# Kernel optimization log

Hardware: AMD Instinct MI355X
Metric: run time of the kernel (lower is better)

Reference implementation:

```python
import jax, jax.numpy as jnp
import numpy as np

H = 1024      # hidden_size
NH = 16       # num_attention_heads
HD = H // NH  # attention_head_size = 64
B, S = 2, 2048


def setup_inputs() -> dict:
    key = jax.random.key(0)
    ks = jax.random.split(key, 8)
    scale = 1.0 / np.sqrt(H)
    return {
        "hidden_states": jax.random.normal(ks[0], (B, S, H), dtype=jnp.float32),
        "attention_mask": jnp.zeros((B, 1, 1, S), dtype=jnp.float32),
        "Wq": jax.random.normal(ks[1], (H, H), dtype=jnp.float32) * scale,
        "bq": jax.random.normal(ks[2], (H,), dtype=jnp.float32) * 0.02,
        "Wk": jax.random.normal(ks[3], (H, H), dtype=jnp.float32) * scale,
        "bk": jax.random.normal(ks[4], (H,), dtype=jnp.float32) * 0.02,
        "Wv": jax.random.normal(ks[5], (H, H), dtype=jnp.float32) * scale,
        "bv": jax.random.normal(ks[6], (H,), dtype=jnp.float32) * 0.02,
    }


def _split_heads(x):
    # [B,S,H] -> [B,NH,S,HD]
    b, s, _ = x.shape
    return x.reshape(b, s, NH, HD).transpose(0, 2, 1, 3)


def reference(hidden_states, attention_mask, Wq, bq, Wk, bk, Wv, bv):
    q = _split_heads(hidden_states @ Wq.T + bq)  # [B,NH,S,HD]
    k = _split_heads(hidden_states @ Wk.T + bk)
    v = _split_heads(hidden_states @ Wv.T + bv)
    scores = jnp.einsum("bhqd,bhkd->bhqk", q, k) / np.sqrt(HD).astype(np.float32)
    scores = scores + attention_mask  # additive mask, broadcast over heads/queries
    weights = jax.nn.softmax(scores, axis=-1)  # dropout is identity in eval mode
    ctx = jnp.einsum("bhqk,bhkd->bhqd", weights, v)  # [B,NH,S,HD]
    return ctx.transpose(0, 2, 1, 3).reshape(hidden_states.shape[0], hidden_states.shape[1], H)
```

## Files before the change

kernel.cpp:

```cpp
#include <hip/hip_runtime.h>
#include <hip/hip_bf16.h>
#include <math.h>

#define HSZ   1024
#define NHEAD 16
#define HDIM  64
#define BATCH 2
#define SEQ   2048

#define LOG2E 1.4426950408889634f

typedef __attribute__((ext_vector_type(8))) short short8;
typedef __attribute__((ext_vector_type(4))) short short4_t;
typedef __attribute__((ext_vector_type(4))) float floatx4;

typedef __attribute__((address_space(1))) const unsigned int gu32;
typedef __attribute__((address_space(3))) unsigned int lu32;

__device__ __forceinline__ void g2lds16(const void* g, void* l) {
    __builtin_amdgcn_global_load_lds((gu32*)g, (lu32*)l, 16, 0, 0);
}

__device__ __forceinline__ short f2bf(float f) {
    union { float f; unsigned u; } v; v.f = f;
    unsigned r = (v.u + 0x7FFF + ((v.u >> 16) & 1)) >> 16;
    return (short)r;
}

__device__ __forceinline__ unsigned pk2(float a, float b) {
    __hip_bfloat162 h = __float22bfloat162_rn(make_float2(a, b));
    return *(unsigned*)&h;
}

__device__ __forceinline__ float ex2(float x) {
#if __has_builtin(__builtin_amdgcn_exp2f)
    return __builtin_amdgcn_exp2f(x);
#else
    return exp2f(x);
#endif
}

#if __has_builtin(__builtin_amdgcn_mfma_f32_16x16x16_bf16)
#define MFMA16(a, b, c) __builtin_amdgcn_mfma_f32_16x16x16_bf16(a, b, c, 0, 0, 0)
#else
#define MFMA16(a, b, c) __builtin_amdgcn_mfma_f32_16x16x16bf16_1k(a, b, c, 0, 0, 0)
#endif

__global__ __launch_bounds__(256) void convert_kernel(
    const float4* __restrict__ X, const float4* __restrict__ Wq,
    const float4* __restrict__ Wk, const float4* __restrict__ Wv,
    const float4* __restrict__ Mask,
    short4_t* __restrict__ Xb, short4_t* __restrict__ Wb,
    float4* __restrict__ Mw)
{
    int idx = blockIdx.x * 256 + threadIdx.x;
    if (idx >= 1835008) {
        int t = idx - 1835008;
        float4 f = Mask[t];
        float4 o;
        o.x = f.x * LOG2E; o.y = f.y * LOG2E;
        o.z = f.z * LOG2E; o.w = f.w * LOG2E;
        Mw[t] = o;
        return;
    }
    const float4* src; short4_t* dst;
    if (idx < 1048576) { src = X + idx; dst = Xb + idx; }
    else {
        int t = idx - 1048576;
        int sel = t >> 18;
        int wi  = t & 0x3FFFF;
        src = (sel == 0 ? Wq : sel == 1 ? Wk : Wv) + wi;
        dst = Wb + (sel << 18) + wi;
    }
    float4 f = *src;
    short4_t o;
    o.x = f2bf(f.x); o.y = f2bf(f.y); o.z = f2bf(f.z); o.w = f2bf(f.w);
    *dst = o;
}

__global__ __launch_bounds__(256, 3) void qkv_mfma_kernel(
    const short* __restrict__ Xb, const short* __restrict__ Wb,
    const float* __restrict__ bq, const float* __restrict__ bk,
    const float* __restrict__ bv,
    short* __restrict__ qo, short* __restrict__ ko, short* __restrict__ vT)
{
    __shared__ short Sm[128 * 136];
    short* As = Sm;
    short* Bs = Sm + 8192;

    const int tid  = threadIdx.x;
    const int lane = tid & 63;
    const int w    = tid >> 6;
    const int l    = lane & 15, quad = lane >> 4;
    const int gM   = blockIdx.y * 128;
    const int gN   = blockIdx.x * 128;
    const int wm   = (w >> 1) * 64, wn = (w & 1) * 64;
    const int ci   = lane >> 3, pb = lane & 7;

    floatx4 acc[4][4] = {};

    for (int kt = 0; kt < HSZ / 64; ++kt) {
        const int k0 = kt * 64;
        __syncthreads();
        #pragma unroll
        for (int u = 0; u < 4; ++u) {
            int c  = w * 4 + u;
            int r  = c * 8 + ci;
            int lb = pb ^ (r & 7);
            g2lds16(Xb + (size_t)(gM + r) * HSZ + k0 + lb * 8, &As[c * 512]);
            g2lds16(Wb + (size_t)(gN + r) * HSZ + k0 + lb * 8, &Bs[c * 512]);
        }
        __syncthreads();
        #pragma unroll
        for (int kk = 0; kk < 2; ++kk) {
            short8 a[4], b[4];
            #pragma unroll
            for (int i = 0; i < 4; ++i) {
                int m = wm + i * 16 + l;
                a[i] = *(const short8*)&As[m * 64 + (((quad + kk * 4) ^ (m & 7)) << 3)];
                int n = wn + i * 16 + l;
                b[i] = *(const short8*)&Bs[n * 64 + (((quad + kk * 4) ^ (n & 7)) << 3)];
            }
            #pragma unroll
            for (int i = 0; i < 4; ++i)
                #pragma unroll
                for (int j = 0; j < 4; ++j)
                    acc[i][j] = __builtin_amdgcn_mfma_f32_16x16x32_bf16(
                        a[i], b[j], acc[i][j], 0, 0, 0);
        }
    }

    const int mat = gN >> 10;
    const int bb = gM >> 11, ss0 = gM & (SEQ - 1);

    if (mat == 2) {
        __syncthreads();
        #pragma unroll
        for (int j = 0; j < 4; ++j) {
            int fl = wn + j * 16 + l;
            float bv_ = bv[(gN & 1023) + fl];
            #pragma unroll
            for (int i = 0; i < 4; ++i)
                #pragma unroll
                for (int r = 0; r < 4; ++r)
                    Sm[fl * 136 + wm + i * 16 + quad * 4 + r]
                        = f2bf(acc[i][j][r] + bv_);
        }
        __syncthreads();
        #pragma unroll
        for (int it = 0; it < 16; ++it) {
            int f = (tid >> 5) + it * 8;
            int c = (tid & 31) * 4;
            short4_t val = *(const short4_t*)&Sm[f * 136 + c];
            int nft = (gN & 1023) + f;
            int head = nft >> 6, d = nft & 63;
            *(short4_t*)&vT[(((size_t)(bb * NHEAD + head)) * HDIM + d) * SEQ
                            + ss0 + c] = val;
        }
        return;
    }

    const float* bias = (mat == 0) ? bq : bk;
    short* dst        = (mat == 0) ? qo : ko;
    const float qscale = (mat == 0) ? 0.125f * LOG2E : 1.0f;

    __syncthreads();
    #pragma unroll
    for (int j = 0; j < 4; ++j) {
        int fl = wn + j * 16 + l;
        float bb_ = bias[(gN & 1023) + fl];
        #pragma unroll
        for (int i = 0; i < 4; ++i)
            #pragma unroll
            for (int r = 0; r < 4; ++r)
                Sm[(wm + i * 16 + quad * 4 + r) * 136 + fl]
                    = f2bf((acc[i][j][r] + bb_) * qscale);
    }
    __syncthreads();
    #pragma unroll
    for (int it = 0; it < 8; ++it) {
        int row = (tid >> 4) + it * 16;
        int fc  = (tid & 15) * 8;
        short8 val = *(const short8*)&Sm[row * 136 + fc];
        int nft = (gN & 1023) + fc;
        int head = nft >> 6, d = nft & 63;
        *(short8*)&dst[(((size_t)(bb * NHEAD + head)) * SEQ + ss0 + row) * HDIM + d]
            = val;
    }
}

__global__ __launch_bounds__(256, 3) void attn_kernel(
    const short* __restrict__ Qg, const short* __restrict__ Kg,
    const short* __restrict__ VTg, const float* __restrict__ maskw,
    float* __restrict__ out)
{
    __shared__ alignas(16) short Sh[4][4096];
    __shared__ alignas(16) float Ms[2][64];
    __shared__ alignas(16) float Lx[4][4][16];

    const int tid  = threadIdx.x;
    const int lane = tid & 63;
    const int kh   = tid >> 6;
    const int l    = lane & 15, quad = lane >> 4;
    const int idx  = blockIdx.x;
    const int bh   = idx & 31;
    const int qt   = idx >> 5;
    const int batch = bh >> 4, head = bh & 15;
    const int ci = lane >> 3, pb = lane & 7;

    const short* Qb = Qg + ((size_t)bh * SEQ + qt * 64) * HDIM;
    const short* Kb = Kg + (size_t)bh * SEQ * HDIM;
    const short* Vb = VTg + (size_t)bh * HDIM * SEQ;
    const float* mrow = maskw + (size_t)batch * SEQ;

    short* Qst = (short*)&Sh[2][0];

    #pragma unroll
    for (int u = 0; u < 2; ++u) {
        int c = kh * 2 + u;
        int r = c * 8 + ci;
        int lb = pb ^ (r & 7);
        g2lds16(Qb + (size_t)r * HDIM + lb * 8, &Qst[c * 512]);
        g2lds16(Kb + (size_t)r * HDIM + lb * 8, &Sh[0][c * 512]);
        g2lds16(Vb + (size_t)r * SEQ + lb * 8, &Sh[1][c * 512]);
    }
    if (tid < 16) g2lds16(mrow + tid * 4, &Ms[0][0]);
    __syncthreads();

    short8 aq[4][2];
    #pragma unroll
    for (int n = 0; n < 4; ++n)
        #pragma unroll
        for (int kk = 0; kk < 2; ++kk) {
            int m = n * 16 + l;
            aq[n][kk] = *(const short8*)&Qst[m * 64
                          + (((quad + kk * 4) ^ (m & 7)) << 3)];
        }
    __syncthreads();

    #pragma unroll
    for (int u = 0; u < 2; ++u) {
        int c = kh * 2 + u;
        int r = c * 8 + ci;
        int lb = pb ^ (r & 7);
        g2lds16(Kb + (size_t)(64 + r) * HDIM + lb * 8, &Sh[2][c * 512]);
        g2lds16(Vb + (size_t)r * SEQ + 64 + lb * 8, &Sh[3][c * 512]);
    }
    if (tid < 16) g2lds16(mrow + 64 + tid * 4, &Ms[1][0]);

    const int akoff0 = (kh * 16 + l) * 64 + (((quad + 0) ^ ((kh * 16 + l) & 7)) << 3);
    const int akoff1 = (kh * 16 + l) * 64 + (((quad + 4) ^ ((kh * 16 + l) & 7)) << 3);
    const int blog   = kh * 2 + (quad >> 1);
    const int bhalf  = (quad & 1) * 4;

    short8 ak0 = *(const short8*)&Sh[0][akoff0];
    short8 ak1 = *(const short8*)&Sh[0][akoff1];
    short4_t bvf[4];
    #pragma unroll
    for (int nd = 0; nd < 4; ++nd) {
        int d = nd * 16 + l;
        bvf[nd] = *(const short4_t*)&Sh[1][d * 64 + ((blog ^ (d & 7)) << 3) + bhalf];
    }
    floatx4 s[4];
    {
        float4 mq = *(const float4*)&Ms[0][kh * 16 + quad * 4];
        floatx4 ini = {mq.x, mq.y, mq.z, mq.w};
        #pragma unroll
        for (int n = 0; n < 4; ++n) s[n] = ini;
        #pragma unroll
        for (int n = 0; n < 4; ++n) {
            s[n] = __builtin_amdgcn_mfma_f32_16x16x32_bf16(ak0, aq[n][0], s[n], 0, 0, 0);
            s[n] = __builtin_amdgcn_mfma_f32_16x16x32_bf16(ak1, aq[n][1], s[n], 0, 0, 0);
        }
    }

    floatx4 o[4][4] = {};
    float l_i[4] = {0.f, 0.f, 0.f, 0.f};

    for (int t = 0; t < 32; ++t) {
        short4_t ap[4];
        #pragma unroll
        for (int n = 0; n < 4; ++n) {
            s[n][0] = ex2(s[n][0]);
            s[n][1] = ex2(s[n][1]);
            s[n][2] = ex2(s[n][2]);
            s[n][3] = ex2(s[n][3]);
            l_i[n] += (s[n][0] + s[n][1]) + (s[n][2] + s[n][3]);
            union { unsigned u[2]; short4_t s4; } pu;
            pu.u[0] = pk2(s[n][0], s[n][1]);
            pu.u[1] = pk2(s[n][2], s[n][3]);
            ap[n] = pu.s4;
        }
        #pragma unroll
        for (int nq = 0; nq < 4; ++nq)
            #pragma unroll
            for (int nd = 0; nd < 4; ++nd)
                o[nq][nd] = MFMA16(ap[nq], bvf[nd], o[nq][nd]);

        if (t < 31) {
            __syncthreads();
            if (t < 30) {
                const int r0 = (t + 2) * 64;
                const int bd = t & 1;
                #pragma unroll
                for (int u = 0; u < 2; ++u) {
                    int c = kh * 2 + u;
                    int r = c * 8 + ci;
                    int lb = pb ^ (r & 7);
                    g2lds16(Kb + (size_t)(r0 + r) * HDIM + lb * 8,
                            &Sh[2 * bd][c * 512]);
                    g2lds16(Vb + (size_t)r * SEQ + r0 + lb * 8,
                            &Sh[2 * bd + 1][c * 512]);
                }
                if (tid < 16) g2lds16(mrow + r0 + tid * 4, &Ms[t & 1][0]);
            }
            const int bb = (t + 1) & 1;
            ak0 = *(const short8*)&Sh[2 * bb][akoff0];
            ak1 = *(const short8*)&Sh[2 * bb][akoff1];
            #pragma unroll
            for (int nd = 0; nd < 4; ++nd) {
                int d = nd * 16 + l;
                bvf[nd] = *(const short4_t*)&Sh[2 * bb + 1]
                              [d * 64 + ((blog ^ (d & 7)) << 3) + bhalf];
            }
            float4 mq = *(const float4*)&Ms[bb][kh * 16 + quad * 4];
            floatx4 ini = {mq.x, mq.y, mq.z, mq.w};
            #pragma unroll
            for (int n = 0; n < 4; ++n) s[n] = ini;
            #pragma unroll
            for (int n = 0; n < 4; ++n) {
                s[n] = __builtin_amdgcn_mfma_f32_16x16x32_bf16(ak0, aq[n][0], s[n], 0, 0, 0);
                s[n] = __builtin_amdgcn_mfma_f32_16x16x32_bf16(ak1, aq[n][1], s[n], 0, 0, 0);
            }
        }
    }

    #pragma unroll
    for (int n = 0; n < 4; ++n) {
        float v = l_i[n];
        v += __shfl_xor(v, 16);
        v += __shfl_xor(v, 32);
        l_i[n] = v;
    }
    float* r0buf = (float*)&Sh[0][0];
    float* r1buf = (float*)&Sh[2][0];
    __syncthreads();
    if (kh != 0 && lane < 16) {
        #pragma unroll
        for (int n = 0; n < 4; ++n) Lx[kh][n][lane] = l_i[n];
    }
    if (kh == 1 || kh == 3) {
        float* dstb = (kh == 1) ? r0buf : r1buf;
        #pragma unroll
        for (int nq = 0; nq < 4; ++nq)
            #pragma unroll
            for (int nd = 0; nd < 4; ++nd)
                *(floatx4*)&dstb[((nq * 4 + nd) * 64 + lane) * 4] = o[nq][nd];
    }
    __syncthreads();
    if (kh == 0 || kh == 2) {
        const float* srcb = (kh == 0) ? r0buf : r1buf;
        #pragma unroll
        for (int nq = 0; nq < 4; ++nq)
            #pragma unroll
            for (int nd = 0; nd < 4; ++nd)
                o[nq][nd] += *(const floatx4*)&srcb[((nq * 4 + nd) * 64 + lane) * 4];
    }
    __syncthreads();
    if (kh == 2) {
        #pragma unroll
        for (int nq = 0; nq < 4; ++nq)
            #pragma unroll
            for (int nd = 0; nd < 4; ++nd)
                *(floatx4*)&r0buf[((nq * 4 + nd) * 64 + lane) * 4] = o[nq][nd];
    }
    __syncthreads();
    if (kh == 0) {
        #pragma unroll
        for (int nq = 0; nq < 4; ++nq)
            #pragma unroll
            for (int nd = 0; nd < 4; ++nd)
                o[nq][nd] += *(const floatx4*)&r0buf[((nq * 4 + nd) * 64 + lane) * 4];
        float lf[4];
        #pragma unroll
        for (int n = 0; n < 4; ++n)
            lf[n] = l_i[n] + Lx[1][n][l] + Lx[2][n][l] + Lx[3][n][l];
        #pragma unroll
        for (int nq = 0; nq < 4; ++nq) {
            #pragma unroll
            for (int r = 0; r < 4; ++r) {
                float inv = 1.0f / __shfl(lf[nq], (lane & 48) + quad * 4 + r);
                int qrow = qt * 64 + nq * 16 + quad * 4 + r;
                #pragma unroll
                for (int nd = 0; nd < 4; ++nd)
                    out[((size_t)batch * SEQ + qrow) * HSZ + head * HDIM + nd * 16 + l]
                        = o[nq][nd][r] * inv;
            }
        }
    }
}

extern "C" void kernel_launch(void* const* d_in, const int* in_sizes, int n_in,
                              void* d_out, int out_size, void* d_ws, size_t ws_size,
                              hipStream_t stream) {
    const float* hs   = (const float*)d_in[0];
    const float* mask = (const float*)d_in[1];
    const float* Wq   = (const float*)d_in[2];
    const float* bq   = (const float*)d_in[3];
    const float* Wk   = (const float*)d_in[4];
    const float* bk   = (const float*)d_in[5];
    const float* Wv   = (const float*)d_in[6];
    const float* bv   = (const float*)d_in[7];
    float* out = (float*)d_out;

    short* Xb = (short*)d_ws;
    short* Wb = Xb + 4194304;
    short* qb = Wb + 3145728;
    short* kb = qb + 4194304;
    short* vT = kb + 4194304;
    float* Mw = (float*)(vT + 4194304);

    convert_kernel<<<7172, 256, 0, stream>>>(
        (const float4*)hs, (const float4*)Wq, (const float4*)Wk, (const float4*)Wv,
        (const float4*)mask, (short4_t*)Xb, (short4_t*)Wb, (float4*)Mw);

    dim3 g2(3 * HSZ / 128, BATCH * SEQ / 128);
    qkv_mfma_kernel<<<g2, 256, 0, stream>>>(Xb, Wb, bq, bk, bv, qb, kb, vT);

    attn_kernel<<<1024, 256, 0, stream>>>(qb, kb, vT, Mw, out);
}
```

Before: 173.6 us.

## Load K/V fragments directly from global into registers, dropping LDS staging

Removes the LDS double-buffered staging of K, V and mask tiles along with the per-iteration block barrier. Each wave now loads its own MFMA operand fragments straight from global memory into registers, prefetching the next tile one iteration ahead. This cuts barrier and LDS traffic but replaces wide coalesced 16-byte async copies with narrower, strided per-lane global loads, notably the short4 V^T loads that stride by SEQ. LDS now holds only the final cross-wave reduction buffer.

```diff
diff --git a/kernel.cpp b/kernel.cpp
--- a/kernel.cpp
+++ b/kernel.cpp
@@ -194,8 +194,7 @@
     const short* __restrict__ VTg, const float* __restrict__ maskw,
     float* __restrict__ out)
 {
-    __shared__ alignas(16) short Sh[4][4096];
-    __shared__ alignas(16) float Ms[2][64];
+    __shared__ alignas(16) float Cb[2][4096];
     __shared__ alignas(16) float Lx[4][4][16];
 
     const int tid  = threadIdx.x;
@@ -206,78 +205,58 @@
     const int bh   = idx & 31;
     const int qt   = idx >> 5;
     const int batch = bh >> 4, head = bh & 15;
-    const int ci = lane >> 3, pb = lane & 7;
 
     const short* Qb = Qg + ((size_t)bh * SEQ + qt * 64) * HDIM;
     const short* Kb = Kg + (size_t)bh * SEQ * HDIM;
     const short* Vb = VTg + (size_t)bh * HDIM * SEQ;
     const float* mrow = maskw + (size_t)batch * SEQ;
 
-    short* Qst = (short*)&Sh[2][0];
-
-    #pragma unroll
-    for (int u = 0; u < 2; ++u) {
-        int c = kh * 2 + u;
-        int r = c * 8 + ci;
-        int lb = pb ^ (r & 7);
-        g2lds16(Qb + (size_t)r * HDIM + lb * 8, &Qst[c * 512]);
-        g2lds16(Kb + (size_t)r * HDIM + lb * 8, &Sh[0][c * 512]);
-        g2lds16(Vb + (size_t)r * SEQ + lb * 8, &Sh[1][c * 512]);
-    }
-    if (tid < 16) g2lds16(mrow + tid * 4, &Ms[0][0]);
-    __syncthreads();
-
     short8 aq[4][2];
     #pragma unroll
     for (int n = 0; n < 4; ++n)
         #pragma unroll
-        for (int kk = 0; kk < 2; ++kk) {
-            int m = n * 16 + l;
-            aq[n][kk] = *(const short8*)&Qst[m * 64
-                          + (((quad + kk * 4) ^ (m & 7)) << 3)];
-        }
-    __syncthreads();
-
-    #pragma unroll
-    for (int u = 0; u < 2; ++u) {
-        int c = kh * 2 + u;
-        int r = c * 8 + ci;
-        int lb = pb ^ (r & 7);
-        g2lds16(Kb + (size_t)(64 + r) * HDIM + lb * 8, &Sh[2][c * 512]);
-        g2lds16(Vb + (size_t)r * SEQ + 64 + lb * 8, &Sh[3][c * 512]);
-    }
-    if (tid < 16) g2lds16(mrow + 64 + tid * 4, &Ms[1][0]);
-
-    const int akoff0 = (kh * 16 + l) * 64 + (((quad + 0) ^ ((kh * 16 + l) & 7)) << 3);
-    const int akoff1 = (kh * 16 + l) * 64 + (((quad + 4) ^ ((kh * 16 + l) & 7)) << 3);
-    const int blog   = kh * 2 + (quad >> 1);
-    const int bhalf  = (quad & 1) * 4;
-
-    short8 ak0 = *(const short8*)&Sh[0][akoff0];
-    short8 ak1 = *(const short8*)&Sh[0][akoff1];
+        for (int kk = 0; kk < 2; ++kk)
+            aq[n][kk] = *(const short8*)&Qb[(n * 16 + l) * 64 + kk * 32 + quad * 8];
+
+    const short* kp = Kb + (kh * 16 + l) * 64 + quad * 8;
+    const short* vp = Vb + (size_t)l * SEQ + kh * 16 + quad * 4;
+    const float* mp = mrow + kh * 16 + quad * 4;
+
+    floatx4 o[4][4] = {};
+    float l_i[4] = {0.f, 0.f, 0.f, 0.f};
+
+    short8 ak0 = *(const short8*)kp;
+    short8 ak1 = *(const short8*)(kp + 32);
     short4_t bvf[4];
     #pragma unroll
-    for (int nd = 0; nd < 4; ++nd) {
-        int d = nd * 16 + l;
-        bvf[nd] = *(const short4_t*)&Sh[1][d * 64 + ((blog ^ (d & 7)) << 3) + bhalf];
-    }
-    floatx4 s[4];
-    {
-        float4 mq = *(const float4*)&Ms[0][kh * 16 + quad * 4];
-        floatx4 ini = {mq.x, mq.y, mq.z, mq.w};
-        #pragma unroll
-        for (int n = 0; n < 4; ++n) s[n] = ini;
+    for (int nd = 0; nd < 4; ++nd)
+        bvf[nd] = *(const short4_t*)(vp + (size_t)nd * 16 * SEQ);
+    float4 mq = *(const float4*)mp;
+
+    for (int t = 0; t < 32; ++t) {
+        kp += 4096; vp += 64; mp += 64;
+        short8 nak0, nak1; short4_t nbv[4]; float4 nmq;
+        if (t < 31) {
+            nak0 = *(const short8*)kp;
+            nak1 = *(const short8*)(kp + 32);
+            #pragma unroll
+            for (int nd = 0; nd < 4; ++nd)
+                nbv[nd] = *(const short4_t*)(vp + (size_t)nd * 16 * SEQ);
+            nmq = *(const float4*)mp;
+        }
+
+        floatx4 s[4];
+        {
+            floatx4 ini = {mq.x, mq.y, mq.z, mq.w};
+            #pragma unroll
+            for (int n = 0; n < 4; ++n) s[n] = ini;
+        }
         #pragma unroll
         for (int n = 0; n < 4; ++n) {
             s[n] = __builtin_amdgcn_mfma_f32_16x16x32_bf16(ak0, aq[n][0], s[n], 0, 0, 0);
             s[n] = __builtin_amdgcn_mfma_f32_16x16x32_bf16(ak1, aq[n][1], s[n], 0, 0, 0);
         }
-    }
-
-    floatx4 o[4][4] = {};
-    float l_i[4] = {0.f, 0.f, 0.f, 0.f};
-
-    for (int t = 0; t < 32; ++t) {
+
         short4_t ap[4];
         #pragma unroll
         for (int n = 0; n < 4; ++n) {
@@ -297,42 +276,10 @@
             for (int nd = 0; nd < 4; ++nd)
                 o[nq][nd] = MFMA16(ap[nq], bvf[nd], o[nq][nd]);
 
-        if (t < 31) {
-            __syncthreads();
-            if (t < 30) {
-                const int r0 = (t + 2) * 64;
-                const int bd = t & 1;
-                #pragma unroll
-                for (int u = 0; u < 2; ++u) {
-                    int c = kh * 2 + u;
-                    int r = c * 8 + ci;
-                    int lb = pb ^ (r & 7);
-                    g2lds16(Kb + (size_t)(r0 + r) * HDIM + lb * 8,
-                            &Sh[2 * bd][c * 512]);
-                    g2lds16(Vb + (size_t)r * SEQ + r0 + lb * 8,
-                            &Sh[2 * bd + 1][c * 512]);
-                }
-                if (tid < 16) g2lds16(mrow + r0 + tid * 4, &Ms[t & 1][0]);
-            }
-            const int bb = (t + 1) & 1;
-            ak0 = *(const short8*)&Sh[2 * bb][akoff0];
-            ak1 = *(const short8*)&Sh[2 * bb][akoff1];
-            #pragma unroll
-            for (int nd = 0; nd < 4; ++nd) {
-                int d = nd * 16 + l;
-                bvf[nd] = *(const short4_t*)&Sh[2 * bb + 1]
-                              [d * 64 + ((blog ^ (d & 7)) << 3) + bhalf];
-            }
-            float4 mq = *(const float4*)&Ms[bb][kh * 16 + quad * 4];
-            floatx4 ini = {mq.x, mq.y, mq.z, mq.w};
-            #pragma unroll
-            for (int n = 0; n < 4; ++n) s[n] = ini;
-            #pragma unroll
-            for (int n = 0; n < 4; ++n) {
-                s[n] = __builtin_amdgcn_mfma_f32_16x16x32_bf16(ak0, aq[n][0], s[n], 0, 0, 0);
-                s[n] = __builtin_amdgcn_mfma_f32_16x16x32_bf16(ak1, aq[n][1], s[n], 0, 0, 0);
-            }
-        }
+        ak0 = nak0; ak1 = nak1;
+        #pragma unroll
+        for (int nd = 0; nd < 4; ++nd) bvf[nd] = nbv[nd];
+        mq = nmq;
     }
 
     #pragma unroll
@@ -342,15 +289,12 @@
         v += __shfl_xor(v, 32);
         l_i[n] = v;
     }
-    float* r0buf = (float*)&Sh[0][0];
-    float* r1buf = (float*)&Sh[2][0];
-    __syncthreads();
     if (kh != 0 && lane < 16) {
         #pragma unroll
         for (int n = 0; n < 4; ++n) Lx[kh][n][lane] = l_i[n];
     }
     if (kh == 1 || kh == 3) {
-        float* dstb = (kh == 1) ? r0buf : r1buf;
+        float* dstb = (kh == 1) ? Cb[0] : Cb[1];
         #pragma unroll
         for (int nq = 0; nq < 4; ++nq)
             #pragma unroll
@@ -359,7 +303,7 @@
     }
     __syncthreads();
     if (kh == 0 || kh == 2) {
-        const float* srcb = (kh == 0) ? r0buf : r1buf;
+        const float* srcb = (kh == 0) ? Cb[0] : Cb[1];
         #pragma unroll
         for (int nq = 0; nq < 4; ++nq)
             #pragma unroll
@@ -372,7 +316,7 @@
         for (int nq = 0; nq < 4; ++nq)
             #pragma unroll
             for (int nd = 0; nd < 4; ++nd)
-                *(floatx4*)&r0buf[((nq * 4 + nd) * 64 + lane) * 4] = o[nq][nd];
+                *(floatx4*)&Cb[0][((nq * 4 + nd) * 64 + lane) * 4] = o[nq][nd];
     }
     __syncthreads();
     if (kh == 0) {
@@ -380,7 +324,7 @@
         for (int nq = 0; nq < 4; ++nq)
             #pragma unroll
             for (int nd = 0; nd < 4; ++nd)
-                o[nq][nd] += *(const floatx4*)&r0buf[((nq * 4 + nd) * 64 + lane) * 4];
+                o[nq][nd] += *(const floatx4*)&Cb[0][((nq * 4 + nd) * 64 + lane) * 4];
         float lf[4];
         #pragma unroll
         for (int n = 0; n < 4; ++n)
```

Measured after the change: 210.8 us. 1.21x slower.
